# Kernel tuning notes

Measured on AMD Instinct MI355X. Metric: run time of the kernel, lower is better.

## Reference

```python
import jax, jax.numpy as jnp
import numpy as np

DG = 8      # deformable groups
K = 3       # deform kernel size
K2 = K * K
CPG = 64 // DG  # input channels per deformable group


def conv2d(x, w, b, pad):
    out = jax.lax.conv_general_dilated(
        x, w, window_strides=(1, 1), padding=[(pad, pad), (pad, pad)],
        dimension_numbers=('NCHW', 'OIHW', 'NCHW'))
    return out + b[None, :, None, None]


def resize_axis(x, out_len, axis):
    # PyTorch bilinear, align_corners=False (half-pixel centers, src clamped >= 0)
    in_len = x.shape[axis]
    src = (jnp.arange(out_len, dtype=jnp.float32) + 0.5) * (in_len / out_len) - 0.5
    src = jnp.maximum(src, 0.0)
    i0 = jnp.floor(src).astype(jnp.int32)
    i1 = jnp.minimum(i0 + 1, in_len - 1)
    t = src - i0.astype(jnp.float32)
    a = jnp.take(x, i0, axis=axis)
    c = jnp.take(x, i1, axis=axis)
    shp = [1] * x.ndim
    shp[axis] = out_len
    t = t.reshape(shp)
    return a * (1.0 - t) + c * t


def bilinear_resize(x, H, W):
    return resize_axis(resize_axis(x, H, 2), W, 3)


def modulated_deform_conv(y, off, msk, w, b):
    # y: [B,C,H,W]; off: [B,DG*2*K2,H,W] (per kernel pt: dy then dx);
    # msk: [B,DG*K2,H,W]; w: [O,C,K,K]; stride=1, pad=K//2, dilation=1.
    B, C, H, W = y.shape
    off = off.reshape(B, DG, K2, 2, H, W)
    off_y, off_x = off[:, :, :, 0], off[:, :, :, 1]      # [B,DG,K2,H,W]
    msk = msk.reshape(B, DG, K2, H, W)

    ky, kx = jnp.meshgrid(jnp.arange(K), jnp.arange(K), indexing='ij')
    kdy = (ky.reshape(-1) - K // 2).astype(jnp.float32)  # kernel y displacement
    kdx = (kx.reshape(-1) - K // 2).astype(jnp.float32)
    hh = jnp.arange(H, dtype=jnp.float32)[:, None]
    ww = jnp.arange(W, dtype=jnp.float32)[None, :]
    py = hh[None, None, None] + kdy[None, None, :, None, None] + off_y  # [B,DG,K2,H,W]
    px = ww[None, None, None] + kdx[None, None, :, None, None] + off_x

    y0 = jnp.floor(py)
    x0 = jnp.floor(px)
    ty = py - y0
    tx = px - x0
    y0i = y0.astype(jnp.int32)
    x0i = x0.astype(jnp.int32)

    yg = y.reshape(B, DG, CPG, H * W)

    def gather(yi, xi):
        valid = ((yi >= 0) & (yi < H) & (xi >= 0) & (xi < W)).astype(y.dtype)
        idx = jnp.clip(yi, 0, H - 1) * W + jnp.clip(xi, 0, W - 1)  # [B,DG,K2,H,W]
        idxf = jnp.broadcast_to(idx.reshape(B, DG, 1, K2 * H * W),
                                (B, DG, CPG, K2 * H * W))
        v = jnp.take_along_axis(yg, idxf, axis=3).reshape(B, DG, CPG, K2, H, W)
        return v * valid[:, :, None]

    v00 = gather(y0i, x0i)
    v01 = gather(y0i, x0i + 1)
    v10 = gather(y0i + 1, x0i)
    v11 = gather(y0i + 1, x0i + 1)

    wy = ty[:, :, None]  # [B,DG,1,K2,H,W]
    wx = tx[:, :, None]
    val = (v00 * (1 - wy) * (1 - wx) + v01 * (1 - wy) * wx
           + v10 * wy * (1 - wx) + v11 * wy * wx)
    val = val * msk[:, :, None]

    wk = w.reshape(w.shape[0], DG, CPG, K2)  # [O,DG,CPG,K2]
    out = jnp.einsum('bgckhw,ogck->bohw', val, wk) + b[None, :, None, None]
    return out


def setup_inputs() -> dict:
    key = jax.random.key(0)
    ks = jax.random.split(key, 6)
    in_nc, out_nc, deform_nc = 64, 64, 64
    om_ch = DG * 3 * K2  # 216
    x = jax.random.normal(ks[0], (4, in_nc, 48, 48), dtype=jnp.float32)
    y = jax.random.normal(ks[1], (4, deform_nc, 96, 96), dtype=jnp.float32)
    w_om = jax.random.normal(ks[2], (om_ch, in_nc, 3, 3), dtype=jnp.float32) * 0.04
    b_om = jax.random.normal(ks[3], (om_ch,), dtype=jnp.float32) * 0.04
    w_dc = jax.random.normal(ks[4], (out_nc, deform_nc, K, K), dtype=jnp.float32) * 0.04
    b_dc = jax.random.normal(ks[5], (out_nc,), dtype=jnp.float32) * 0.04
    return {"x": x, "y": y, "w_om": w_om, "b_om": b_om, "w_dc": w_dc, "b_dc": b_dc}


def reference(x, y, w_om, b_om, w_dc, b_dc):
    B, _, Hy, Wy = y.shape
    off_msk = conv2d(x, w_om, b_om, pad=1)                 # [B,DG*3*K2,Hx,Wx]
    off_msk = bilinear_resize(off_msk, Hy, Wy)             # to y's spatial size
    off = off_msk[:, :DG * 2 * K2]
    msk = jax.nn.sigmoid(off_msk[:, DG * 2 * K2:])
    return jax.nn.relu(modulated_deform_conv(y, off, msk, w_dc, b_dc))
```

## Files before the change

kernel.cpp:

```cpp
#include <hip/hip_runtime.h>
#include <math.h>

#define HX 48
#define WX 48
#define OMC 216
#define HY 96
#define WY 96

typedef __attribute__((ext_vector_type(8))) short bf16x8;
typedef __attribute__((ext_vector_type(4))) float f32x4;

__device__ inline unsigned short f2bf(float f) {
  unsigned u = __float_as_uint(f);
  return (unsigned short)((u + 0x7fffu + ((u >> 16) & 1u)) >> 16);
}
__device__ inline unsigned pk2(float a, float b) {
  return (unsigned)f2bf(a) | ((unsigned)f2bf(b) << 16);
}
#define B2F(u) __uint_as_float((unsigned)(u) << 16)


__global__ __launch_bounds__(256) void prep_ytr_kernel(
    const float* __restrict__ w_om, const float* __restrict__ w_dc,
    const float* __restrict__ y,
    unsigned short* __restrict__ ap2, unsigned short* __restrict__ ap1,
    unsigned short* __restrict__ ytbf) {
  __shared__ float tile[64][65];
  int bid = blockIdx.x;
  int t = threadIdx.x;
  if (bid < 720) {
    int idx = bid * 256 + t;
    if (idx < 147456) {
      int j = idx & 7;
      int tmp = idx >> 3;
      int l = tmp & 63; tmp >>= 6;
      int m = tmp & 15; tmp >>= 4;
      int s = tmp % 6, p = tmp / 6;
      int oc = m * 16 + (l & 15);
      int kk = s * 32 + (l >> 4) * 8 + j;
      int tap = kk >> 6, c = kk & 63;
      int k = p * 3 + tap;
      ap2[idx] = (oc < OMC) ? f2bf(w_om[oc * 576 + c * 9 + k]) : (unsigned short)0;
    } else {
      int i2 = idx - 147456;
      int j = i2 & 7;
      int tmp = i2 >> 3;
      int l = tmp & 63; tmp >>= 6;
      int w = tmp & 3; tmp >>= 2;
      int s = tmp % 6, p = tmp / 6;
      int oc = w * 16 + (l & 15);
      int kk = s * 32 + (l >> 4) * 8 + j;
      int tap = kk >> 6, c = kk & 63;
      ap1[i2] = f2bf(w_dc[oc * 576 + c * 9 + p * 3 + tap]);
    }
  } else {
    int blk = bid - 720;
    int b = blk / 144;
    int p0 = (blk % 144) * 64;
    int pl = t & 63;
    int cb = t >> 6;
#pragma unroll
    for (int i = 0; i < 16; ++i) {
      int c = cb * 16 + i;
      tile[c][pl] = y[((size_t)(b * 64 + c)) * 9216 + p0 + pl];
    }
    __syncthreads();
    int cw = t & 63;
    int pb = t >> 6;
#pragma unroll
    for (int i = 0; i < 16; ++i) {
      int p = pb * 16 + i;
      ytbf[((size_t)((b * 8 + (cw >> 3)) * 9216) + p0 + p) * 8 + (cw & 7)] =
          f2bf(tile[cw][p]);
    }
  }
}

__global__ __launch_bounds__(256) void conv_mfma_kernel(
    const float* __restrict__ x, const unsigned short* __restrict__ ap2,
    const float* __restrict__ bom, float* __restrict__ om) {
  __shared__ unsigned short sB[9][16][72];
  int t = threadIdx.x;
  int bid = blockIdx.x;
  int logical = (bid & 7) * 144 + (bid >> 3);
  int och = logical / 576;
  int rem = logical % 576;
  int b = rem / 144;
  int tl = rem % 144;
  int h0 = (tl / 12) * 4;
  int w0 = (tl % 12) * 4;
  int s_ic = t >> 2;
  int s_row = t & 3;
  const float* xp = x + (size_t)b * 64 * 2304 + (size_t)s_ic * 2304;

  float4 X[3][3];
  bool hvr[3];
#pragma unroll
  for (int r = 0; r < 3; ++r) {
    int hh = h0 + s_row + r - 1;
    hvr[r] = (unsigned)hh < (unsigned)HX;
    int hc = min(max(hh, 0), HX - 1);
    const float* xr = xp + hc * WX;
#pragma unroll
    for (int q = 0; q < 3; ++q) {
      int cb = min(max(w0 - 4 + 4 * q, 0), WX - 4);
      X[r][q] = *(const float4*)&xr[cb];
    }
  }
#pragma unroll
  for (int k = 0; k < 9; ++k) {
    int dy = k / 3 - 1, dx = k % 3 - 1;
    int r = dy + 1;
#pragma unroll
    for (int j = 0; j < 4; ++j) {
      int idx = j + dx + 4;
      int q = idx >> 2, e = idx & 3;
      float val = (e == 0) ? X[r][q].x : (e == 1) ? X[r][q].y
                : (e == 2) ? X[r][q].z : X[r][q].w;
      bool cv = (unsigned)(w0 + j + dx) < (unsigned)WX;
      float v = (hvr[r] && cv) ? val : 0.f;
      sB[k][s_row * 4 + j][s_ic] = f2bf(v);
    }
  }
  __syncthreads();

  int w = t >> 6;
  int l = t & 63;
  int lr = l & 15;
  int lg = l >> 4;
  f32x4 acc[2] = {};
#pragma unroll
  for (int p = 0; p < 3; ++p) {
#pragma unroll
    for (int s = 0; s < 6; ++s) {
      int tapidx = p * 3 + (s >> 1);
      int c0 = (s & 1) * 32;
      bf16x8 bv = *(const bf16x8*)&sB[tapidx][lr][c0 + lg * 8];
#pragma unroll
      for (int m = 0; m < 2; ++m) {
        int mq = och * 8 + w * 2 + m;
        bf16x8 av = *(const bf16x8*)(ap2 +
            (size_t)((((p * 6 + s) * 16) + mq) * 64 + l) * 8);
        acc[m] = __builtin_amdgcn_mfma_f32_16x16x32_bf16(av, bv, acc[m], 0, 0, 0);
      }
    }
  }
  int prow = lr >> 2, pcol = lr & 3;
#pragma unroll
  for (int m = 0; m < 2; ++m) {
    int ocb = (och * 8 + w * 2 + m) * 16 + lg * 4;
    if (ocb < OMC) {
      float4 bb = *(const float4*)&bom[ocb];
      float bvv[4] = {bb.x, bb.y, bb.z, bb.w};
#pragma unroll
      for (int i = 0; i < 4; ++i) {
        om[((size_t)(b * OMC + ocb + i)) * 2304 + (h0 + prow) * WX + w0 + pcol] =
            acc[m][i] + bvv[i];
      }
    }
  }
}

__global__ __launch_bounds__(256) void deform_mfma_kernel(
    const unsigned short* __restrict__ ytbf, const float* __restrict__ om,
    const unsigned short* __restrict__ ap1, const float* __restrict__ bdc,
    float* __restrict__ out) {
  __shared__ float sTy[72][16];
  __shared__ float sTx[72][16];
  __shared__ float sTm[72][16];
  __shared__ unsigned short sval[2][16][72];
  int t = threadIdx.x;
  int bid = blockIdx.x;
  int logical = (bid & 7) * 288 + (bid >> 3);
  int b = logical / 576;
  int tl = logical % 576;
  int h0 = (tl / 24) * 4;
  int w0 = (tl % 24) * 4;
  const float* omb = om + (size_t)b * OMC * 2304;

#pragma unroll
  for (int r = 0; r < 5; ++r) {
    int j = t + r * 256;
    if (j < 1152) {
      int k = j >> 7;
      int g = (j >> 4) & 7;
      int px = j & 15;
      int gh = h0 + (px >> 2);
      int gw = w0 + (px & 3);
      float sh = fmaxf(gh * 0.5f - 0.25f, 0.f);
      float sw = fmaxf(gw * 0.5f - 0.25f, 0.f);
      int i0h = (int)sh; float th = sh - (float)i0h;
      int i0w = (int)sw; float tw = sw - (float)i0w;
      int i1h = min(i0h + 1, HX - 1);
      int i1w = min(i0w + 1, WX - 1);
      float r00 = (1.f - th) * (1.f - tw), r01 = (1.f - th) * tw;
      float r10 = th * (1.f - tw),         r11 = th * tw;
      int a00 = i0h * WX + i0w, a01 = i0h * WX + i1w;
      int a10 = i1h * WX + i0w, a11 = i1h * WX + i1w;
      const float* cy = omb + (size_t)(g * 18 + k * 2) * 2304;
      const float* cx = cy + 2304;
      const float* cm = omb + (size_t)(144 + g * 9 + k) * 2304;
      float oy = r00 * cy[a00] + r01 * cy[a01] + r10 * cy[a10] + r11 * cy[a11];
      float ox = r00 * cx[a00] + r01 * cx[a01] + r10 * cx[a10] + r11 * cx[a11];
      float mv = r00 * cm[a00] + r01 * cm[a01] + r10 * cm[a10] + r11 * cm[a11];
      int row = k * 8 + g;
      sTy[row][px] = (float)(gh + k / 3 - 1) + oy;
      sTx[row][px] = (float)(gw + k % 3 - 1) + ox;
      sTm[row][px] = 1.f / (1.f + __expf(-mv));
    }
  }

  int item = t >> 1;
  int g = item >> 4;
  int px = item & 15;
  int cp = t & 1;
  int chb = g * 8 + cp * 4;
  const unsigned short* ytg =
      ytbf + ((size_t)((logical / 576) * 8 + g) * 9216) * 8 + cp * 4;

  int w = t >> 6;
  int l = t & 63;
  int lr = l & 15;
  int lg = l >> 4;

  __syncthreads();

  ushort4 U[2][4];
  float W[2][4];

  auto issueC = [&](int k, ushort4* Uo, float* Wo) {
    int row = k * 8 + g;
    float py = sTy[row][px], pxf = sTx[row][px], m = sTm[row][px];
    float y0f = floorf(py), x0f = floorf(pxf);
    float ty = py - y0f, tx = pxf - x0f;
    int y0 = (int)y0f, x0 = (int)x0f;
    int y1 = y0 + 1, x1 = x0 + 1;
    float w00 = (1.f - ty) * (1.f - tx) * m, w01 = (1.f - ty) * tx * m;
    float w10 = ty * (1.f - tx) * m,         w11 = ty * tx * m;
    Wo[0] = ((unsigned)y0 < HY && (unsigned)x0 < WY) ? w00 : 0.f;
    Wo[1] = ((unsigned)y0 < HY && (unsigned)x1 < WY) ? w01 : 0.f;
    Wo[2] = ((unsigned)y1 < HY && (unsigned)x0 < WY) ? w10 : 0.f;
    Wo[3] = ((unsigned)y1 < HY && (unsigned)x1 < WY) ? w11 : 0.f;
    int y0c = min(max(y0, 0), HY - 1), y1c = min(max(y1, 0), HY - 1);
    int x0c = min(max(x0, 0), WY - 1), x1c = min(max(x1, 0), WY - 1);
    Uo[0] = *(const ushort4*)(ytg + ((size_t)(y0c * WY + x0c) << 3));
    Uo[1] = *(const ushort4*)(ytg + ((size_t)(y0c * WY + x1c) << 3));
    Uo[2] = *(const ushort4*)(ytg + ((size_t)(y1c * WY + x0c) << 3));
    Uo[3] = *(const ushort4*)(ytg + ((size_t)(y1c * WY + x1c) << 3));
  };
  auto finishC = [&](const ushort4* Ui, const float* Wi, int buf) {
    float4 s0 = {0.f, 0.f, 0.f, 0.f};
#pragma unroll
    for (int c4 = 0; c4 < 4; ++c4) {
      float wgt = Wi[c4];
      s0.x += wgt * B2F(Ui[c4].x);
      s0.y += wgt * B2F(Ui[c4].y);
      s0.z += wgt * B2F(Ui[c4].z);
      s0.w += wgt * B2F(Ui[c4].w);
    }
    *(uint2*)&sval[buf][px][chb] = make_uint2(pk2(s0.x, s0.y), pk2(s0.z, s0.w));
  };

  issueC(0, U[0], W[0]);
  __builtin_amdgcn_sched_barrier(0);

  f32x4 acc = {};
#pragma unroll
  for (int tp = 0; tp < 9; ++tp) {
    if (tp + 1 < 9) {
      issueC(tp + 1, U[(tp + 1) & 1], W[(tp + 1) & 1]);
      __builtin_amdgcn_sched_barrier(0);
    }
    finishC(U[tp & 1], W[tp & 1], tp & 1);
    __syncthreads();
    int p = tp / 3;
    int sl = (tp % 3) * 2;
#pragma unroll
    for (int half = 0; half < 2; ++half) {
      int s = sl + half;
      bf16x8 av = *(const bf16x8*)(ap1 +
          (size_t)(((p * 6 + s) * 4 + w) * 64 + l) * 8);
      bf16x8 bv = *(const bf16x8*)&sval[tp & 1][lr][half * 32 + lg * 8];
      acc = __builtin_amdgcn_mfma_f32_16x16x32_bf16(av, bv, acc, 0, 0, 0);
    }
  }

  float4 bb = *(const float4*)&bdc[w * 16 + lg * 4];
  float bvv[4] = {bb.x, bb.y, bb.z, bb.w};
#pragma unroll
  for (int i = 0; i < 4; ++i) {
    int oc = w * 16 + lg * 4 + i;
    out[((size_t)(b * 64 + oc) * 96 + h0 + (lr >> 2)) * 96 + w0 + (lr & 3)] =
        fmaxf(acc[i] + bvv[i], 0.f);
  }
}

extern "C" void kernel_launch(void* const* d_in, const int* in_sizes, int n_in,
                              void* d_out, int out_size, void* d_ws, size_t ws_size,
                              hipStream_t stream) {
  const float* x = (const float*)d_in[0];
  const float* y = (const float*)d_in[1];
  const float* w_om = (const float*)d_in[2];
  const float* b_om = (const float*)d_in[3];
  const float* w_dc = (const float*)d_in[4];
  const float* b_dc = (const float*)d_in[5];
  float* out = (float*)d_out;

  float* om  = (float*)d_ws;
  unsigned short* ap2 = (unsigned short*)(om + 1990656);
  unsigned short* ap1 = ap2 + 147456;
  unsigned short* ytbf = ap1 + 36864;

  prep_ytr_kernel<<<1296, 256, 0, stream>>>(w_om, w_dc, y, ap2, ap1, ytbf);
  conv_mfma_kernel<<<1152, 256, 0, stream>>>(x, ap2, b_om, om);
  deform_mfma_kernel<<<2304, 256, 0, stream>>>(ytbf, om, ap1, b_dc, out);
}
```

Baseline: 57.32 us.

## Relayout bf16 y into 4-channel planes to fetch horizontal corner pairs in one load

```diff
diff --git a/kernel.cpp b/kernel.cpp
--- a/kernel.cpp
+++ b/kernel.cpp
@@ -8,6 +8,7 @@
 #define WY 96
 
 typedef __attribute__((ext_vector_type(8))) short bf16x8;
+typedef __attribute__((ext_vector_type(8))) unsigned short ushort8;
 typedef __attribute__((ext_vector_type(4))) float f32x4;
 
 __device__ inline unsigned short f2bf(float f) {
@@ -70,7 +71,7 @@
 #pragma unroll
     for (int i = 0; i < 16; ++i) {
       int p = pb * 16 + i;
-      ytbf[((size_t)((b * 8 + (cw >> 3)) * 9216) + p0 + p) * 8 + (cw & 7)] =
+      ytbf[((size_t)((b * 16 + (cw >> 2)) * 9216) + p0 + p) * 4 + (cw & 3)] =
           f2bf(tile[cw][p]);
     }
   }
@@ -216,7 +217,7 @@
   int cp = t & 1;
   int chb = g * 8 + cp * 4;
   const unsigned short* ytg =
-      ytbf + ((size_t)((logical / 576) * 8 + g) * 9216) * 8 + cp * 4;
+      ytbf + (size_t)((b * 16 + g * 2 + cp) * 9216) * 4;
 
   int w = t >> 6;
   int l = t & 63;
@@ -225,10 +226,10 @@
 
   __syncthreads();
 
-  ushort4 U[2][4];
+  ushort8 U[2][2];
   float W[2][4];
 
-  auto issueC = [&](int k, ushort4* Uo, float* Wo) {
+  auto issueC = [&](int k, ushort8* Uo, float* Wo) {
     int row = k * 8 + g;
     float py = sTy[row][px], pxf = sTx[row][px], m = sTm[row][px];
     float y0f = floorf(py), x0f = floorf(pxf);
@@ -237,27 +238,31 @@
     int y1 = y0 + 1, x1 = x0 + 1;
     float w00 = (1.f - ty) * (1.f - tx) * m, w01 = (1.f - ty) * tx * m;
     float w10 = ty * (1.f - tx) * m,         w11 = ty * tx * m;
-    Wo[0] = ((unsigned)y0 < HY && (unsigned)x0 < WY) ? w00 : 0.f;
-    Wo[1] = ((unsigned)y0 < HY && (unsigned)x1 < WY) ? w01 : 0.f;
-    Wo[2] = ((unsigned)y1 < HY && (unsigned)x0 < WY) ? w10 : 0.f;
-    Wo[3] = ((unsigned)y1 < HY && (unsigned)x1 < WY) ? w11 : 0.f;
+    bool xv0 = (unsigned)x0 < (unsigned)WY, xv1 = (unsigned)x1 < (unsigned)WY;
+    bool yv0 = (unsigned)y0 < (unsigned)HY, yv1 = (unsigned)y1 < (unsigned)HY;
+    int xb = min(max(x0, 0), WY - 2);
+    int i0 = x0 - xb;
+    bool s0n = (i0 == 0), sm1 = (i0 == -1), sp1 = (i0 == 1);
+    float wa0 = xv0 ? w00 : 0.f, wb0 = xv1 ? w01 : 0.f;
+    float wa1 = xv0 ? w10 : 0.f, wb1 = xv1 ? w11 : 0.f;
+    Wo[0] = yv0 ? (s0n ? wa0 : (sm1 ? wb0 : 0.f)) : 0.f;
+    Wo[1] = yv0 ? (s0n ? wb0 : (sp1 ? wa0 : 0.f)) : 0.f;
+    Wo[2] = yv1 ? (s0n ? wa1 : (sm1 ? wb1 : 0.f)) : 0.f;
+    Wo[3] = yv1 ? (s0n ? wb1 : (sp1 ? wa1 : 0.f)) : 0.f;
     int y0c = min(max(y0, 0), HY - 1), y1c = min(max(y1, 0), HY - 1);
-    int x0c = min(max(x0, 0), WY - 1), x1c = min(max(x1, 0), WY - 1);
-    Uo[0] = *(const ushort4*)(ytg + ((size_t)(y0c * WY + x0c) << 3));
-    Uo[1] = *(const ushort4*)(ytg + ((size_t)(y0c * WY + x1c) << 3));
-    Uo[2] = *(const ushort4*)(ytg + ((size_t)(y1c * WY + x0c) << 3));
-    Uo[3] = *(const ushort4*)(ytg + ((size_t)(y1c * WY + x1c) << 3));
+    Uo[0] = *(const ushort8*)(ytg + ((size_t)(y0c * WY + xb) << 2));
+    Uo[1] = *(const ushort8*)(ytg + ((size_t)(y1c * WY + xb) << 2));
   };
-  auto finishC = [&](const ushort4* Ui, const float* Wi, int buf) {
-    float4 s0 = {0.f, 0.f, 0.f, 0.f};
-#pragma unroll
-    for (int c4 = 0; c4 < 4; ++c4) {
-      float wgt = Wi[c4];
-      s0.x += wgt * B2F(Ui[c4].x);
-      s0.y += wgt * B2F(Ui[c4].y);
-      s0.z += wgt * B2F(Ui[c4].z);
-      s0.w += wgt * B2F(Ui[c4].w);
-    }
+  auto finishC = [&](const ushort8* Ui, const float* Wi, int buf) {
+    float4 s0;
+    s0.x = Wi[0] * B2F(Ui[0][0]) + Wi[1] * B2F(Ui[0][4]) +
+           Wi[2] * B2F(Ui[1][0]) + Wi[3] * B2F(Ui[1][4]);
+    s0.y = Wi[0] * B2F(Ui[0][1]) + Wi[1] * B2F(Ui[0][5]) +
+           Wi[2] * B2F(Ui[1][1]) + Wi[3] * B2F(Ui[1][5]);
+    s0.z = Wi[0] * B2F(Ui[0][2]) + Wi[1] * B2F(Ui[0][6]) +
+           Wi[2] * B2F(Ui[1][2]) + Wi[3] * B2F(Ui[1][6]);
+    s0.w = Wi[0] * B2F(Ui[0][3]) + Wi[1] * B2F(Ui[0][7]) +
+           Wi[2] * B2F(Ui[1][3]) + Wi[3] * B2F(Ui[1][7]);
     *(uint2*)&sval[buf][px][chb] = make_uint2(pk2(s0.x, s0.y), pk2(s0.z, s0.w));
   };
 
```

New measurement: 60.64 us. 5.8% more time.
